# Kernel tuning notes

Hardware: AMD Instinct MI355X
Metric: run time of the kernel (lower is better)

## Reference

```python
import jax, jax.numpy as jnp
import numpy as np

B, N, D, C, NCLS = 8, 2048, 256, 128, 50
EPS = 1e-5  # BatchNorm eps

def _bn(x, g, b):
    # eval-mode BatchNorm1d over channel dim of (B,C,N): running_mean=0, running_var=1
    return x * (g / jnp.sqrt(1.0 + EPS))[:, None] + b[:, None]

def _complex_linear(x, Wr, br, Wi, bi):
    # torch ComplexLinear: complex(fr(x.real)-fi(x.imag), fr(x.imag)+fi(x.real))
    xr, xi = x.real, x.imag
    re = (xr @ Wr.T + br) - (xi @ Wi.T + bi)
    im = (xi @ Wr.T + br) + (xr @ Wi.T + bi)
    return jax.lax.complex(re, im)

def _sa(x, qkW, vW, vb, tW, tb, g, b):
    # x: (B,C,N); q/k share weights (tied in torch), dim C//4
    xq = jnp.einsum('qc,bcn->bnq', qkW, x)            # (B,N,C/4)
    xk = jnp.einsum('qc,bcm->bqm', qkW, x)            # (B,C/4,N)
    energy = jnp.einsum('bnq,bqm->bnm', xq, xk)       # (B,N,N)
    attn = jax.nn.softmax(energy, axis=-1)
    attn = attn / (1e-9 + attn.sum(axis=1, keepdims=True))  # column renorm
    xv = jnp.einsum('oc,bcn->bon', vW, x) + vb[:, None]
    xr = x - jnp.einsum('bcn,bnm->bcm', xv, attn)
    xr = jnp.einsum('oc,bcn->bon', tW, xr) + tb[:, None]
    return x + jax.nn.relu(_bn(xr, g, b))

def reference(xyz, cls_label, A, Bmat, W1r, b1r, W1i, b1i, W2r, b2r, W2i, b2i,
              lbl_emb, ft_w1, ft_g1, ft_b1, ft_w2, ft_g2, ft_b2,
              sa_qk, sa_vw, sa_vb, sa_tw, sa_tb, sa_g, sa_b,
              fuse_w, fuse_g, fuse_b, c1_w, c1_b, bn1_g, bn1_b, c2_w, c2_b):
    pts = xyz.transpose(0, 2, 1)                       # (B,N,3)
    # VecKM(d=256, alpha=30, beta=9): G = eB (eB^H eA), normalized to sqrt(d)
    eA = jnp.exp(1j * (pts @ A))                       # (B,N,D) complex64
    eB = jnp.exp(1j * (pts @ Bmat))
    inner = jnp.einsum('bnd,bne->bde', eB.conj(), eA)  # (B,D,D)
    G = jnp.einsum('bnd,bde->bne', eB, inner)          # (B,N,D)
    G = G / jnp.linalg.norm(G, axis=-1, keepdims=True) * jnp.sqrt(jnp.float32(D))
    G = _complex_linear(G, W1r, b1r, W1i, b1i)
    G = jax.lax.complex(jax.nn.relu(G.real), jax.nn.relu(G.imag))  # ComplexReLU
    G = _complex_linear(G, W2r, b2r, W2i, b2i)
    G = (G.real ** 2 + G.imag ** 2).transpose(0, 2, 1)  # (B,D,N)
    reweight = (cls_label @ lbl_emb)[:, :, None]        # (B,D,1)
    x = G * reweight
    x = jax.nn.relu(_bn(jnp.einsum('oc,bcn->bon', ft_w1, x), ft_g1, ft_b1))
    x = _bn(jnp.einsum('oc,bcn->bon', ft_w2, x), ft_g2, ft_b2)  # (B,C,N)
    feats = []
    for i in range(4):
        x = _sa(x, sa_qk[i], sa_vw[i], sa_vb[i], sa_tw[i], sa_tb[i], sa_g[i], sa_b[i])
        feats.append(x)
    x = jnp.concatenate(feats, axis=1)                  # (B,4C,N)
    x = jax.nn.relu(_bn(jnp.einsum('oc,bcn->bon', fuse_w, x), fuse_g, fuse_b))
    x = jax.nn.relu(_bn(jnp.einsum('oc,bcn->bon', c1_w, x) + c1_b[:, None], bn1_g, bn1_b))
    # dropout is identity in eval mode
    x = jnp.einsum('oc,bcn->bon', c2_w, x) + c2_b[:, None]
    x = jax.nn.log_softmax(x, axis=1)
    return x.transpose(0, 2, 1)                         # (B,N,NCLS)

def setup_inputs():
    key = jax.random.key(0)
    k = jax.random.split(key, 24)
    rn = lambda i, s: jax.random.normal(k[i], s, jnp.float32)
    s = 0.05
    return {
        'xyz': rn(0, (B, 3, N)),
        'cls_label': jax.random.uniform(k[1], (B, 16), jnp.float32),
        'A': rn(2, (3, D)) * 30.0,
        'Bmat': rn(3, (3, D)) * 9.0,
        'W1r': rn(4, (D, D)) * s, 'b1r': rn(5, (D,)) * s,
        'W1i': rn(6, (D, D)) * s, 'b1i': rn(7, (D,)) * s,
        'W2r': rn(8, (D, D)) * s, 'b2r': rn(9, (D,)) * s,
        'W2i': rn(10, (D, D)) * s, 'b2i': rn(11, (D,)) * s,
        'lbl_emb': rn(12, (16, D)),
        'ft_w1': rn(13, (C, D)) * s, 'ft_g1': jnp.ones((C,)), 'ft_b1': jnp.zeros((C,)),
        'ft_w2': rn(14, (C, C)) * s, 'ft_g2': jnp.ones((C,)), 'ft_b2': jnp.zeros((C,)),
        'sa_qk': rn(15, (4, C // 4, C)) * s,
        'sa_vw': rn(16, (4, C, C)) * s, 'sa_vb': rn(17, (4, C)) * s,
        'sa_tw': rn(18, (4, C, C)) * s, 'sa_tb': rn(19, (4, C)) * s,
        'sa_g': jnp.ones((4, C)), 'sa_b': jnp.zeros((4, C)),
        'fuse_w': rn(20, (C, 4 * C)) * s, 'fuse_g': jnp.ones((C,)), 'fuse_b': jnp.zeros((C,)),
        'c1_w': rn(21, (C, C)) * s, 'c1_b': rn(22, (C,)) * s,
        'bn1_g': jnp.ones((C,)), 'bn1_b': jnp.zeros((C,)),
        'c2_w': rn(23, (NCLS, C)) * s, 'c2_b': jnp.zeros((NCLS,)),
    }
```

## Files before the change

### kernel.cpp

```cpp
#include <hip/hip_runtime.h>

#define BB 8
#define NPTS 2048
#define DD 256
#define CCH 128
#define NCLASS 50
#define LOG2E 1.4426950408889634f

typedef __attribute__((ext_vector_type(8))) short short8;
typedef __attribute__((ext_vector_type(4))) float f32x4;
typedef unsigned short u16;
#define MFMA16(a,b,c) __builtin_amdgcn_mfma_f32_16x16x32_bf16(a,b,c,0,0,0)

__device__ __forceinline__ u16 f2bf(float x){
  union { float f; unsigned int u; } v; v.f = x;
  unsigned int r = v.u + 0x7FFFu + ((v.u >> 16) & 1u);
  return (u16)(r >> 16);
}
__device__ __forceinline__ float bf2f(u16 u){
  union { unsigned int u32; float f; } v; v.u32 = ((unsigned int)u) << 16; return v.f;
}
__device__ __forceinline__ void split2(float x, u16& h, u16& l){
  h = f2bf(x); l = f2bf(x - bf2f(h));
}
__device__ __forceinline__ short8 ld8(const u16* p){ return *(const short8*)p; }
__device__ __forceinline__ short8 zero8(){ short8 z = {0,0,0,0,0,0,0,0}; return z; }

struct WSplit {
  const float* src[12];
  int cnt[12];
  int off[12];
};
__global__ __launch_bounds__(256) void wsplit_kernel(WSplit wsp, u16* __restrict__ H,
                                                     u16* __restrict__ L)
{
  int seg = blockIdx.y;
  int idx = blockIdx.x*256 + threadIdx.x;
  if (idx >= wsp.cnt[seg]) return;
  float v = wsp.src[seg][idx];
  u16 h, l; split2(v, h, l);
  H[wsp.off[seg]+idx] = h; L[wsp.off[seg]+idx] = l;
}

__global__ __launch_bounds__(256) void ek1_kernel(
    const float* __restrict__ xyz, const float* __restrict__ A, const float* __restrict__ Bm,
    u16* __restrict__ ATrh, u16* __restrict__ ATrl, u16* __restrict__ ATih, u16* __restrict__ ATil,
    u16* __restrict__ BTrh, u16* __restrict__ BTrl, u16* __restrict__ BTih, u16* __restrict__ BTil)
{
  size_t idx = (size_t)blockIdx.x*256 + threadIdx.x;
  int n = (int)(idx & (NPTS-1));
  int d = (int)((idx >> 11) & (DD-1));
  int b = (int)(idx >> 19);
  float p0 = xyz[((size_t)b*3+0)*NPTS+n];
  float p1 = xyz[((size_t)b*3+1)*NPTS+n];
  float p2 = xyz[((size_t)b*3+2)*NPTS+n];
  float phA = p0*A[d] + p1*A[DD+d] + p2*A[2*DD+d];
  float phB = p0*Bm[d] + p1*Bm[DD+d] + p2*Bm[2*DD+d];
  float sa, ca, sb, cb;
  sincosf(phA, &sa, &ca);
  sincosf(phB, &sb, &cb);
  size_t off = ((size_t)b*DD + d)*NPTS + n;
  u16 h, l;
  split2(ca, h, l); ATrh[off] = h; ATrl[off] = l;
  split2(sa, h, l); ATih[off] = h; ATil[off] = l;
  split2(cb, h, l); BTrh[off] = h; BTrl[off] = l;
  split2(sb, h, l); BTih[off] = h; BTil[off] = l;
}

__global__ __launch_bounds__(256) void ek2_kernel(
    const float* __restrict__ xyz, const float* __restrict__ Bm,
    u16* __restrict__ Brh, u16* __restrict__ Brl, u16* __restrict__ Bih, u16* __restrict__ Bil)
{
  size_t idx = (size_t)blockIdx.x*256 + threadIdx.x;
  int d = (int)(idx & (DD-1));
  int n = (int)((idx >> 8) & (NPTS-1));
  int b = (int)(idx >> 19);
  float p0 = xyz[((size_t)b*3+0)*NPTS+n];
  float p1 = xyz[((size_t)b*3+1)*NPTS+n];
  float p2 = xyz[((size_t)b*3+2)*NPTS+n];
  float phB = p0*Bm[d] + p1*Bm[DD+d] + p2*Bm[2*DD+d];
  float sb, cb;
  sincosf(phB, &sb, &cb);
  size_t off = ((size_t)b*NPTS + n)*DD + d;
  u16 h, l;
  split2(cb, h, l); Brh[off] = h; Brl[off] = l;
  split2(sb, h, l); Bih[off] = h; Bil[off] = l;
}

__global__ __launch_bounds__(256) void inner_mfma_kernel(
    const u16* __restrict__ ATrh, const u16* __restrict__ ATrl,
    const u16* __restrict__ ATih, const u16* __restrict__ ATil,
    const u16* __restrict__ BTrh, const u16* __restrict__ BTrl,
    const u16* __restrict__ BTih, const u16* __restrict__ BTil,
    float2* __restrict__ PART)
{
  int z = blockIdx.z; int b = z & 7; int ch = z >> 3;
  int e0 = blockIdx.y*64, d0 = blockIdx.x*64;
  int tid = threadIdx.x, lane = tid & 63, w = tid >> 6;
  int wr = (w >> 1)*32, wc = (w & 1)*32;
  int r16 = lane & 15, g4 = lane >> 4;
  f32x4 re[2][2] = {}, ip[2][2] = {}, iq[2][2] = {};
  size_t ar_[2], br_[2];
  #pragma unroll
  for (int rg = 0; rg < 2; rg++) {
    ar_[rg] = ((size_t)b*DD + (e0 + wr + rg*16 + r16))*NPTS + g4*8;
    br_[rg] = ((size_t)b*DD + (d0 + wc + rg*16 + r16))*NPTS + g4*8;
  }
  int kbeg = ch*512, kend = kbeg + 512;
  for (int k0 = kbeg; k0 < kend; k0 += 32) {
    short8 arh[2], arl[2], aih[2], ail[2], brh[2], brl[2], bih[2], bil[2];
    #pragma unroll
    for (int rg = 0; rg < 2; rg++) {
      arh[rg] = ld8(ATrh + ar_[rg] + k0); arl[rg] = ld8(ATrl + ar_[rg] + k0);
      aih[rg] = ld8(ATih + ar_[rg] + k0); ail[rg] = ld8(ATil + ar_[rg] + k0);
      brh[rg] = ld8(BTrh + br_[rg] + k0); brl[rg] = ld8(BTrl + br_[rg] + k0);
      bih[rg] = ld8(BTih + br_[rg] + k0); bil[rg] = ld8(BTil + br_[rg] + k0);
    }
    #pragma unroll
    for (int ra = 0; ra < 2; ra++)
      #pragma unroll
      for (int rb = 0; rb < 2; rb++) {
        re[ra][rb] = MFMA16(arh[ra], brh[rb], re[ra][rb]);
        re[ra][rb] = MFMA16(arh[ra], brl[rb], re[ra][rb]);
        re[ra][rb] = MFMA16(arl[ra], brh[rb], re[ra][rb]);
        re[ra][rb] = MFMA16(aih[ra], bih[rb], re[ra][rb]);
        re[ra][rb] = MFMA16(aih[ra], bil[rb], re[ra][rb]);
        re[ra][rb] = MFMA16(ail[ra], bih[rb], re[ra][rb]);
        ip[ra][rb] = MFMA16(aih[ra], brh[rb], ip[ra][rb]);
        ip[ra][rb] = MFMA16(aih[ra], brl[rb], ip[ra][rb]);
        ip[ra][rb] = MFMA16(ail[ra], brh[rb], ip[ra][rb]);
        iq[ra][rb] = MFMA16(arh[ra], bih[rb], iq[ra][rb]);
        iq[ra][rb] = MFMA16(arh[ra], bil[rb], iq[ra][rb]);
        iq[ra][rb] = MFMA16(arl[ra], bih[rb], iq[ra][rb]);
      }
  }
  float2* outp = PART + ((size_t)(ch*BB + b)*DD)*DD;
  #pragma unroll
  for (int ra = 0; ra < 2; ra++)
    #pragma unroll
    for (int rb = 0; rb < 2; rb++)
      #pragma unroll
      for (int j = 0; j < 4; j++) {
        int e = e0 + wr + ra*16 + g4*4 + j;
        int d = d0 + wc + rb*16 + r16;
        outp[(size_t)e*DD + d] = make_float2(re[ra][rb][j], ip[ra][rb][j] - iq[ra][rb][j]);
      }
}

__global__ __launch_bounds__(256) void innred_kernel(const float2* __restrict__ P,
    u16* __restrict__ Irh, u16* __restrict__ Irl, u16* __restrict__ Iih, u16* __restrict__ Iil)
{
  size_t i = (size_t)blockIdx.x*256 + threadIdx.x;
  const size_t S = (size_t)BB*DD*DD;
  float2 a = P[i], b = P[i+S], c = P[i+2*S], d = P[i+3*S];
  float rr = a.x+b.x+c.x+d.x, ii = a.y+b.y+c.y+d.y;
  u16 h, l;
  split2(rr, h, l); Irh[i] = h; Irl[i] = l;
  split2(ii, h, l); Iih[i] = h; Iil[i] = l;
}

__global__ __launch_bounds__(256) void g_mfma_kernel(
    const u16* __restrict__ Brh, const u16* __restrict__ Brl,
    const u16* __restrict__ Bih, const u16* __restrict__ Bil,
    const u16* __restrict__ Irh, const u16* __restrict__ Irl,
    const u16* __restrict__ Iih, const u16* __restrict__ Iil,
    float2* __restrict__ G)
{
  int b = blockIdx.z;
  int n0 = blockIdx.y*64, e0 = blockIdx.x*64;
  int tid = threadIdx.x, lane = tid & 63, w = tid >> 6;
  int wr = (w >> 1)*32, wc = (w & 1)*32;
  int r16 = lane & 15, g4 = lane >> 4;
  f32x4 p[2][2] = {}, q[2][2] = {}, im[2][2] = {};
  size_t ar_[2], br_[2];
  #pragma unroll
  for (int rg = 0; rg < 2; rg++) {
    ar_[rg] = ((size_t)b*NPTS + (n0 + wr + rg*16 + r16))*DD + g4*8;
    br_[rg] = ((size_t)b*DD + (e0 + wc + rg*16 + r16))*DD + g4*8;
  }
  for (int k0 = 0; k0 < DD; k0 += 32) {
    short8 arh[2], arl[2], aih[2], ail[2], brh[2], brl[2], bih[2], bil[2];
    #pragma unroll
    for (int rg = 0; rg < 2; rg++) {
      arh[rg] = ld8(Brh + ar_[rg] + k0); arl[rg] = ld8(Brl + ar_[rg] + k0);
      aih[rg] = ld8(Bih + ar_[rg] + k0); ail[rg] = ld8(Bil + ar_[rg] + k0);
      brh[rg] = ld8(Irh + br_[rg] + k0); brl[rg] = ld8(Irl + br_[rg] + k0);
      bih[rg] = ld8(Iih + br_[rg] + k0); bil[rg] = ld8(Iil + br_[rg] + k0);
    }
    #pragma unroll
    for (int ra = 0; ra < 2; ra++)
      #pragma unroll
      for (int rb = 0; rb < 2; rb++) {
        p[ra][rb] = MFMA16(arh[ra], brh[rb], p[ra][rb]);
        p[ra][rb] = MFMA16(arh[ra], brl[rb], p[ra][rb]);
        p[ra][rb] = MFMA16(arl[ra], brh[rb], p[ra][rb]);
        q[ra][rb] = MFMA16(aih[ra], bih[rb], q[ra][rb]);
        q[ra][rb] = MFMA16(aih[ra], bil[rb], q[ra][rb]);
        q[ra][rb] = MFMA16(ail[ra], bih[rb], q[ra][rb]);
        im[ra][rb] = MFMA16(arh[ra], bih[rb], im[ra][rb]);
        im[ra][rb] = MFMA16(arh[ra], bil[rb], im[ra][rb]);
        im[ra][rb] = MFMA16(arl[ra], bih[rb], im[ra][rb]);
        im[ra][rb] = MFMA16(aih[ra], brh[rb], im[ra][rb]);
        im[ra][rb] = MFMA16(aih[ra], brl[rb], im[ra][rb]);
        im[ra][rb] = MFMA16(ail[ra], brh[rb], im[ra][rb]);
      }
  }
  #pragma unroll
  for (int ra = 0; ra < 2; ra++)
    #pragma unroll
    for (int rb = 0; rb < 2; rb++)
      #pragma unroll
      for (int j = 0; j < 4; j++) {
        int n = n0 + wr + ra*16 + g4*4 + j;
        int e = e0 + wc + rb*16 + r16;
        G[((size_t)b*NPTS + n)*DD + e] = make_float2(p[ra][rb][j] - q[ra][rb][j], im[ra][rb][j]);
      }
}

__global__ __launch_bounds__(256) void gnormsplit_kernel(const float2* __restrict__ Gf,
    u16* __restrict__ Grh, u16* __restrict__ Grl, u16* __restrict__ Gih, u16* __restrict__ Gil)
{
  size_t row = blockIdx.x;
  const float2* p = Gf + row*DD;
  int tid = threadIdx.x;
  float2 v = p[tid];
  __shared__ float red[256];
  red[tid] = v.x*v.x + v.y*v.y;
  __syncthreads();
  for (int w = 128; w > 0; w >>= 1) { if (tid < w) red[tid] += red[tid+w]; __syncthreads(); }
  float sc = 16.f * rsqrtf(red[0]);
  size_t off = row*DD + tid;
  u16 h, l;
  split2(v.x*sc, h, l); Grh[off] = h; Grl[off] = l;
  split2(v.y*sc, h, l); Gih[off] = h; Gil[off] = l;
}

__global__ __launch_bounds__(256) void clinear_mfma_kernel(
    const u16* __restrict__ Arh, const u16* __restrict__ Arl,
    const u16* __restrict__ Aih, const u16* __restrict__ Ail,
    const u16* __restrict__ Wrh, const u16* __restrict__ Wrl,
    const u16* __restrict__ Wih, const u16* __restrict__ Wil,
    const float* __restrict__ br, const float* __restrict__ bi,
    u16* __restrict__ Orh, u16* __restrict__ Orl, u16* __restrict__ Oih, u16* __restrict__ Oil,
    const float* __restrict__ RW, float* __restrict__ GSQ, int mode)
{
  int m0 = blockIdx.y*64, o0 = blockIdx.x*64;
  int tid = threadIdx.x, lane = tid & 63, w = tid >> 6;
  int wr = (w >> 1)*32, wc = (w & 1)*32;
  int r16 = lane & 15, g4 = lane >> 4;
  f32x4 p[2][2] = {}, q[2][2] = {}, im[2][2] = {};
  size_t ar_[2], br_[2];
  #pragma unroll
  for (int rg = 0; rg < 2; rg++) {
    ar_[rg] = (size_t)(m0 + wr + rg*16 + r16)*DD + g4*8;
    br_[rg] = (size_t)(o0 + wc + rg*16 + r16)*DD + g4*8;
  }
  for (int k0 = 0; k0 < DD; k0 += 32) {
    short8 arh[2], arl[2], aih[2], ail[2], brh[2], brl[2], bih[2], bil[2];
    #pragma unroll
    for (int rg = 0; rg < 2; rg++) {
      arh[rg] = ld8(Arh + ar_[rg] + k0); arl[rg] = ld8(Arl + ar_[rg] + k0);
      aih[rg] = ld8(Aih + ar_[rg] + k0); ail[rg] = ld8(Ail + ar_[rg] + k0);
      brh[rg] = ld8(Wrh + br_[rg] + k0); brl[rg] = ld8(Wrl + br_[rg] + k0);
      bih[rg] = ld8(Wih + br_[rg] + k0); bil[rg] = ld8(Wil + br_[rg] + k0);
    }
    #pragma unroll
    for (int ra = 0; ra < 2; ra++)
      #pragma unroll
      for (int rb = 0; rb < 2; rb++) {
        p[ra][rb] = MFMA16(arh[ra], brh[rb], p[ra][rb]);
        p[ra][rb] = MFMA16(arh[ra], brl[rb], p[ra][rb]);
        p[ra][rb] = MFMA16(arl[ra], brh[rb], p[ra][rb]);
        q[ra][rb] = MFMA16(aih[ra], bih[rb], q[ra][rb]);
        q[ra][rb] = MFMA16(aih[ra], bil[rb], q[ra][rb]);
        q[ra][rb] = MFMA16(ail[ra], bih[rb], q[ra][rb]);
        im[ra][rb] = MFMA16(arh[ra], bih[rb], im[ra][rb]);
        im[ra][rb] = MFMA16(arh[ra], bil[rb], im[ra][rb]);
        im[ra][rb] = MFMA16(arl[ra], bih[rb], im[ra][rb]);
        im[ra][rb] = MFMA16(aih[ra], brh[rb], im[ra][rb]);
        im[ra][rb] = MFMA16(aih[ra], brl[rb], im[ra][rb]);
        im[ra][rb] = MFMA16(ail[ra], brh[rb], im[ra][rb]);
      }
  }
  #pragma unroll
  for (int ra = 0; ra < 2; ra++)
    #pragma unroll
    for (int rb = 0; rb < 2; rb++) {
      int o = o0 + wc + rb*16 + r16;
      float brv = br[o], biv = bi[o];
      if (mode == 1) {
        #pragma unroll
        for (int j = 0; j < 4; j++) {
          int m = m0 + wr + ra*16 + g4*4 + j;
          float re = fmaxf(p[ra][rb][j] - q[ra][rb][j] + brv - biv, 0.f);
          float iv = fmaxf(im[ra][rb][j] + brv + biv, 0.f);
          size_t off = (size_t)m*DD + o;
          u16 h, l;
          split2(re, h, l); Orh[off] = h; Orl[off] = l;
          split2(iv, h, l); Oih[off] = h; Oil[off] = l;
        }
      } else {
        int mbase = m0 + wr + ra*16 + g4*4;
        int b = mbase >> 11, nb = mbase & (NPTS-1);
        float rwv = RW[(size_t)b*DD + o];
        float4 gv;
        #pragma unroll
        for (int j = 0; j < 4; j++) {
          float re = p[ra][rb][j] - q[ra][rb][j] + brv - biv;
          float iv = im[ra][rb][j] + brv + biv;
          ((float*)&gv)[j] = (re*re + iv*iv) * rwv;
        }
        *(float4*)(GSQ + ((size_t)b*DD + o)*NPTS + nb) = gv;
      }
    }
}

__global__ void rw_kernel(const float* __restrict__ cls, const float* __restrict__ lbl,
                          float* __restrict__ RW)
{
  int b = blockIdx.x; int d = threadIdx.x;
  float s = 0.f;
  #pragma unroll
  for (int k = 0; k < 16; k++) s += cls[b*16+k] * lbl[k*DD+d];
  RW[b*DD+d] = s;
}

__global__ __launch_bounds__(256) void sgemm_kernel(
    const u16* __restrict__ Wh, const u16* __restrict__ Wl,
    const float* __restrict__ X, float* __restrict__ Y,
    const float* __restrict__ RES,
    const float* __restrict__ bias, const float* __restrict__ bng, const float* __restrict__ bnb,
    u16* __restrict__ YBh, u16* __restrict__ YBl, int ybmode,
    int O, int Cin, size_t xbs, size_t ybs, size_t rbs, int flags)
{
  int b = blockIdx.z;
  int n0 = blockIdx.x*64, o0 = blockIdx.y*64;
  const float* x = X + (size_t)b*xbs;
  __shared__ u16 sXh[64][40], sXl[64][40];
  int tid = threadIdx.x, lane = tid & 63, w = tid >> 6;
  int wo = (w >> 1)*32, wn = (w & 1)*32;
  int r16 = lane & 15, g4 = lane >> 4;
  f32x4 acc[2][2] = {};
  int stc = tid >> 3;
  int stn = (tid & 7)*8;
  for (int k0 = 0; k0 < Cin; k0 += 32) {
    const float* px = x + (size_t)(k0+stc)*NPTS + n0 + stn;
    float4 u0 = *(const float4*)px;
    float4 u1 = *(const float4*)(px+4);
    float v[8] = {u0.x,u0.y,u0.z,u0.w,u1.x,u1.y,u1.z,u1.w};
    __syncthreads();
    #pragma unroll
    for (int j = 0; j < 8; j++) {
      u16 h, l; split2(v[j], h, l);
      sXh[stn+j][stc] = h; sXl[stn+j][stc] = l;
    }
    __syncthreads();
    short8 awh[2], awl[2], bxh[2], bxl[2];
    #pragma unroll
    for (int rg = 0; rg < 2; rg++) {
      int orow = o0 + wo + rg*16 + r16;
      if (orow < O) {
        size_t woff = (size_t)orow*Cin + k0 + g4*8;
        awh[rg] = ld8(Wh + woff); awl[rg] = ld8(Wl + woff);
      } else { awh[rg] = zero8(); awl[rg] = zero8(); }
      bxh[rg] = ld8(&sXh[wn + rg*16 + r16][g4*8]);
      bxl[rg] = ld8(&sXl[wn + rg*16 + r16][g4*8]);
    }
    #pragma unroll
    for (int ra = 0; ra < 2; ra++)
      #pragma unroll
      for (int rb = 0; rb < 2; rb++) {
        acc[ra][rb] = MFMA16(awh[ra], bxh[rb], acc[ra][rb]);
        acc[ra][rb] = MFMA16(awh[ra], bxl[rb], acc[ra][rb]);
        acc[ra][rb] = MFMA16(awl[ra], bxh[rb], acc[ra][rb]);
      }
  }
  #pragma unroll
  for (int ra = 0; ra < 2; ra++)
    #pragma unroll
    for (int rb = 0; rb < 2; rb++)
      #pragma unroll
      for (int j = 0; j < 4; j++) {
        int o = o0 + wo + ra*16 + g4*4 + j;
        if (o >= O) continue;
        int n = n0 + wn + rb*16 + r16;
        float v = acc[ra][rb][j];
        if (flags & 1) v += bias[o];
        if (flags & 2) v = v * (bng[o] * rsqrtf(1.f + 1e-5f)) + bnb[o];
        if (flags & 4) v = fmaxf(v, 0.f);
        if (flags & 8) v += RES[(size_t)b*rbs + (size_t)o*NPTS + n];
        if (ybmode == 0) Y[(size_t)b*ybs + (size_t)o*NPTS + n] = v;
        else if (ybmode == 1) YBh[(size_t)b*ybs + (size_t)o*NPTS + n] = f2bf(v);
        else {
          u16 h, l; split2(v, h, l);
          size_t off = ((size_t)b*NPTS + n)*32 + o;
          YBh[off] = h; YBl[off] = l;
        }
      }
}

__global__ __launch_bounds__(256) void sastat_kernel(
    const u16* __restrict__ Qh, const u16* __restrict__ Ql,
    float* __restrict__ PM, float* __restrict__ PS)
{
  int b = blockIdx.z, ch = blockIdx.y;
  int n0 = blockIdx.x*64;
  size_t base = (size_t)b*NPTS*32;
  int tid = threadIdx.x, lane = tid & 63, wid = tid >> 6;
  int r16 = lane & 15, g4 = lane >> 4;
  size_t ao = base + (size_t)(n0 + wid*16 + r16)*32 + g4*8;
  short8 ah = ld8(Qh + ao), al = ld8(Ql + ao);
  float pm[4] = {-3.4e38f,-3.4e38f,-3.4e38f,-3.4e38f};
  float ps[4] = {0.f,0.f,0.f,0.f};
  int mbeg = ch*512, mend = mbeg + 512;
  for (int mt = mbeg; mt < mend; mt += 32) {
    size_t bo0 = base + (size_t)(mt + r16)*32 + g4*8;
    size_t bo1 = bo0 + 16*32;
    short8 bh0 = ld8(Qh+bo0), bl0 = ld8(Ql+bo0);
    short8 bh1 = ld8(Qh+bo1), bl1 = ld8(Ql+bo1);
    f32x4 a0 = {}, a1 = {};
    a0 = MFMA16(ah, bh0, a0); a0 = MFMA16(ah, bl0, a0); a0 = MFMA16(al, bh0, a0);
    a1 = MFMA16(ah, bh1, a1); a1 = MFMA16(ah, bl1, a1); a1 = MFMA16(al, bh1, a1);
    #pragma unroll
    for (int j = 0; j < 4; j++) {
      float v = fmaxf(a0[j], a1[j]);
      float mn = fmaxf(pm[j], v);
      ps[j] = ps[j]*exp2f((pm[j]-mn)*LOG2E)
            + exp2f((a0[j]-mn)*LOG2E) + exp2f((a1[j]-mn)*LOG2E);
      pm[j] = mn;
    }
  }
  #pragma unroll
  for (int j = 0; j < 4; j++) {
    float m = pm[j], s = ps[j];
    #pragma unroll
    for (int d = 1; d < 16; d <<= 1) {
      float om = __shfl_xor(m, d);
      float os = __shfl_xor(s, d);
      float mn = fmaxf(m, om);
      s = s*exp2f((m-mn)*LOG2E) + os*exp2f((om-mn)*LOG2E);
      m = mn;
    }
    if (r16 == 0) {
      int n_ = n0 + wid*16 + g4*4 + j;
      size_t off = ((size_t)ch*BB + b)*NPTS + n_;
      PM[off] = m; PS[off] = s;
    }
  }
}

__global__ __launch_bounds__(256) void saattn_kernel(
    const u16* __restrict__ Qh, const u16* __restrict__ Ql,
    const float* __restrict__ PM, const float* __restrict__ PS,
    u16* __restrict__ AT, float* __restrict__ CSP)
{
  int b = blockIdx.z, ch = blockIdx.y;
  int m0 = blockIdx.x*64;
  size_t base = (size_t)b*NPTS*32;
  u16* at = AT + (size_t)b*NPTS*NPTS;
  __shared__ u16 lds[4][16][40];
  __shared__ float smx[512], srs[512];
  int tid = threadIdx.x, lane = tid & 63, wid = tid >> 6;
  int r16 = lane & 15, g4 = lane >> 4;
  int nbeg = ch*512, nend = nbeg + 512;
  const size_t S = (size_t)BB*NPTS;
  for (int t = tid; t < 512; t += 256) {
    size_t bn = (size_t)b*NPTS + nbeg + t;
    float m0_ = PM[bn], m1 = PM[S+bn], m2 = PM[2*S+bn], m3 = PM[3*S+bn];
    float mxv = fmaxf(fmaxf(m0_,m1), fmaxf(m2,m3));
    float den = PS[bn]*exp2f((m0_-mxv)*LOG2E) + PS[S+bn]*exp2f((m1-mxv)*LOG2E)
              + PS[2*S+bn]*exp2f((m2-mxv)*LOG2E) + PS[3*S+bn]*exp2f((m3-mxv)*LOG2E);
    smx[t] = mxv; srs[t] = 1.f/den;
  }
  __syncthreads();
  size_t ao = base + (size_t)(m0 + wid*16 + r16)*32 + g4*8;
  short8 ah = ld8(Qh + ao), al = ld8(Ql + ao);
  float csum[4] = {0.f,0.f,0.f,0.f};
  int srow = lane >> 2, soct = (lane & 3)*8;
  for (int nt = nbeg; nt < nend; nt += 32) {
    size_t bo0 = base + (size_t)(nt + r16)*32 + g4*8;
    size_t bo1 = bo0 + 16*32;
    short8 bh0 = ld8(Qh+bo0), bl0 = ld8(Ql+bo0);
    short8 bh1 = ld8(Qh+bo1), bl1 = ld8(Ql+bo1);
    f32x4 a0 = {}, a1 = {};
    a0 = MFMA16(ah, bh0, a0); a0 = MFMA16(ah, bl0, a0); a0 = MFMA16(al, bh0, a0);
    a1 = MFMA16(ah, bh1, a1); a1 = MFMA16(ah, bl1, a1); a1 = MFMA16(al, bh1, a1);
    int nl0 = nt - nbeg + r16, nl1 = nl0 + 16;
    float mx0 = smx[nl0], rs0 = srs[nl0], mx1 = smx[nl1], rs1 = srs[nl1];
    #pragma unroll
    for (int j = 0; j < 4; j++) {
      float t0 = exp2f((a0[j]-mx0)*LOG2E)*rs0;
      float t1 = exp2f((a1[j]-mx1)*LOG2E)*rs1;
      csum[j] += t0 + t1;
      lds[wid][g4*4+j][r16] = f2bf(t0);
      lds[wid][g4*4+j][r16+16] = f2bf(t1);
    }
    __syncthreads();
    short8 row = *(const short8*)&lds[wid][srow][soct];
    *(short8*)(at + (size_t)(m0 + wid*16 + srow)*NPTS + nt + soct) = row;
    __syncthreads();
  }
  #pragma unroll
  for (int j = 0; j < 4; j++) {
    float c = csum[j];
    #pragma unroll
    for (int d = 1; d < 16; d <<= 1) c += __shfl_xor(c, d);
    if (r16 == 0) {
      int m_ = m0 + wid*16 + g4*4 + j;
      CSP[((size_t)ch*BB + b)*NPTS + m_] = c;
    }
  }
}

__global__ __launch_bounds__(256) void apply_mfma_kernel(
    const u16* __restrict__ XV, const u16* __restrict__ AT,
    const float* __restrict__ CSP, const float* __restrict__ XRES, size_t res_bs,
    float* __restrict__ OUT)
{
  int b = blockIdx.z;
  int m0 = blockIdx.x*64;
  int c0 = blockIdx.y*64;
  const u16* xv = XV + (size_t)b*CCH*NPTS;
  const u16* at = AT + (size_t)b*NPTS*NPTS;
  __shared__ float scsi[64];
  int tid = threadIdx.x, lane = tid & 63, w = tid >> 6;
  const size_t S = (size_t)BB*NPTS;
  if (tid < 64) {
    size_t bm = (size_t)b*NPTS + m0 + tid;
    float c = CSP[bm] + CSP[S+bm] + CSP[2*S+bm] + CSP[3*S+bm];
    scsi[tid] = 1.f/(1e-9f + c);
  }
  __syncthreads();
  int wc = c0 + (w >> 1)*32, wm = (w & 1)*32;
  int r16 = lane & 15, g4 = lane >> 4;
  f32x4 acc[2][2] = {};
  const u16* pa0 = xv + (size_t)(wc + r16)*NPTS + g4*8;
  const u16* pa1 = pa0 + (size_t)16*NPTS;
  const u16* pb0 = at + (size_t)(m0 + wm + r16)*NPTS + g4*8;
  const u16* pb1 = pb0 + (size_t)16*NPTS;
  for (int k0 = 0; k0 < NPTS; k0 += 32) {
    short8 a0 = ld8(pa0 + k0);
    short8 a1 = ld8(pa1 + k0);
    short8 b0 = ld8(pb0 + k0);
    short8 b1 = ld8(pb1 + k0);
    acc[0][0] = MFMA16(a0, b0, acc[0][0]);
    acc[0][1] = MFMA16(a0, b1, acc[0][1]);
    acc[1][0] = MFMA16(a1, b0, acc[1][0]);
    acc[1][1] = MFMA16(a1, b1, acc[1][1]);
  }
  #pragma unroll
  for (int ca = 0; ca < 2; ca++)
    #pragma unroll
    for (int mb = 0; mb < 2; mb++) {
      int m = m0 + wm + mb*16 + r16;
      float ci = scsi[wm + mb*16 + r16];
      #pragma unroll
      for (int j = 0; j < 4; j++) {
        int c = wc + ca*16 + g4*4 + j;
        float v = XRES[(size_t)b*res_bs + (size_t)c*NPTS + m] - acc[ca][mb][j]*ci;
        OUT[((size_t)b*CCH + c)*NPTS + m] = v;
      }
    }
}

__global__ __launch_bounds__(256) void lsm_kernel(const float* __restrict__ Y,
                                                  float* __restrict__ OUT)
{
  int idx = blockIdx.x*256 + threadIdx.x;
  int b = idx >> 11, n = idx & (NPTS-1);
  const float* p = Y + (size_t)b*NCLASS*NPTS + n;
  float m = -3.4e38f;
  #pragma unroll
  for (int k = 0; k < NCLASS; k++) m = fmaxf(m, p[(size_t)k*NPTS]);
  float s = 0.f;
  #pragma unroll
  for (int k = 0; k < NCLASS; k++) s += expf(p[(size_t)k*NPTS] - m);
  float L = m + logf(s);
  float* o = OUT + (size_t)idx*NCLASS;
  #pragma unroll
  for (int k = 0; k < NCLASS; k++) o[k] = p[(size_t)k*NPTS] - L;
}

extern "C" void kernel_launch(void* const* d_in, const int* in_sizes, int n_in,
                              void* d_out, int out_size, void* d_ws, size_t ws_size,
                              hipStream_t stream)
{
  (void)in_sizes; (void)n_in; (void)out_size; (void)ws_size;
  const float* xyz  = (const float*)d_in[0];
  const float* cls  = (const float*)d_in[1];
  const float* Amat = (const float*)d_in[2];
  const float* Bm   = (const float*)d_in[3];
  const float* W1r  = (const float*)d_in[4];
  const float* b1r  = (const float*)d_in[5];
  const float* W1i  = (const float*)d_in[6];
  const float* b1i  = (const float*)d_in[7];
  const float* W2r  = (const float*)d_in[8];
  const float* b2r  = (const float*)d_in[9];
  const float* W2i  = (const float*)d_in[10];
  const float* b2i  = (const float*)d_in[11];
  const float* lbl  = (const float*)d_in[12];
  const float* ftw1 = (const float*)d_in[13];
  const float* ftg1 = (const float*)d_in[14];
  const float* ftb1 = (const float*)d_in[15];
  const float* ftw2 = (const float*)d_in[16];
  const float* ftg2 = (const float*)d_in[17];
  const float* ftb2 = (const float*)d_in[18];
  const float* saqk = (const float*)d_in[19];
  const float* savw = (const float*)d_in[20];
  const float* savb = (const float*)d_in[21];
  const float* satw = (const float*)d_in[22];
  const float* satb = (const float*)d_in[23];
  const float* sag  = (const float*)d_in[24];
  const float* sab  = (const float*)d_in[25];
  const float* fusew= (const float*)d_in[26];
  const float* fuseg= (const float*)d_in[27];
  const float* fuseb= (const float*)d_in[28];
  const float* c1w  = (const float*)d_in[29];
  const float* c1b  = (const float*)d_in[30];
  const float* bn1g = (const float*)d_in[31];
  const float* bn1b = (const float*)d_in[32];
  const float* c2w  = (const float*)d_in[33];
  const float* c2b  = (const float*)d_in[34];
  float* out = (float*)d_out;

  float* ws = (float*)d_ws;
  const size_t PS  = (size_t)BB*DD*NPTS;
  const size_t ISZ = (size_t)BB*DD*DD;
  u16* U = (u16*)ws;
  u16 *ATrh = U+0*PS, *ATrl = U+1*PS, *ATih = U+2*PS, *ATil = U+3*PS;
  u16 *BTrh = U+4*PS, *BTrl = U+5*PS, *BTih = U+6*PS, *BTil = U+7*PS;
  u16 *Bnrh = U+8*PS, *Bnrl = U+9*PS, *Bnih = U+10*PS, *Bnil = U+11*PS;
  u16 *Irh = U+12*PS, *Irl = U+12*PS+ISZ, *Iih = U+12*PS+2*ISZ, *Iil = U+12*PS+3*ISZ;
  float* gsq = (float*)(U + 12*PS + 4*ISZ);
  float2* PART = (float2*)gsq;
  float2* Gf = (float2*)ws;
  u16 *G1rh = U+4*PS, *G1rl = U+5*PS, *G1ih = U+6*PS, *G1il = U+7*PS;
  u16 *G2rh = U+8*PS, *G2rl = U+9*PS, *G2ih = U+10*PS, *G2il = U+11*PS;
  u16* attnT = (u16*)ws;
  size_t p = (size_t)BB*NPTS*NPTS;
  float* xfeat = ws + p;  p += (size_t)BB*CCH*NPTS;
  float* feats = ws + p;  p += (size_t)BB*4*CCH*NPTS;
  float* xt1   = ws + p;  p += (size_t)BB*CCH*NPTS;
  float* xt2   = ws + p;  p += (size_t)BB*CCH*NPTS;
  float* ybuf  = ws + p;  p += (size_t)BB*NCLASS*NPTS;
  float* rwb   = ws + p;  p += (size_t)BB*DD;
  float* PMb   = ws + p;  p += (size_t)4*BB*NPTS;
  float* PSb   = ws + p;  p += (size_t)4*BB*NPTS;
  float* CSPb  = ws + p;  p += (size_t)4*BB*NPTS;
  u16* xqh = (u16*)(ws + p);
  u16* xql = xqh + (size_t)BB*NPTS*32;
  u16* xvb = xql + (size_t)BB*NPTS*32;
  u16* wpH = xvb + (size_t)BB*CCH*NPTS;
  u16* wpL = wpH + 557056;

  const int o_w1r=0, o_w1i=65536, o_w2r=131072, o_w2i=196608, o_ft1=262144,
            o_ft2=294912, o_qk=311296, o_vw=327680, o_tw=393216, o_fu=458752,
            o_c1=524288, o_c2=540672;
  WSplit wsp;
  const float* srcs[12] = {W1r,W1i,W2r,W2i,ftw1,ftw2,saqk,savw,satw,fusew,c1w,c2w};
  const int cnts[12] = {65536,65536,65536,65536,32768,16384,16384,65536,65536,65536,16384,6400};
  const int offs[12] = {o_w1r,o_w1i,o_w2r,o_w2i,o_ft1,o_ft2,o_qk,o_vw,o_tw,o_fu,o_c1,o_c2};
  for (int i = 0; i < 12; i++) { wsp.src[i]=srcs[i]; wsp.cnt[i]=cnts[i]; wsp.off[i]=offs[i]; }

  wsplit_kernel<<<dim3(256, 12), 256, 0, stream>>>(wsp, wpH, wpL);
  rw_kernel<<<BB, DD, 0, stream>>>(cls, lbl, rwb);
  ek1_kernel<<<(int)(PS/256), 256, 0, stream>>>(xyz, Amat, Bm,
      ATrh, ATrl, ATih, ATil, BTrh, BTrl, BTih, BTil);
  ek2_kernel<<<(int)(PS/256), 256, 0, stream>>>(xyz, Bm, Bnrh, Bnrl, Bnih, Bnil);
  inner_mfma_kernel<<<dim3(DD/64, DD/64, BB*4), 256, 0, stream>>>(
      ATrh, ATrl, ATih, ATil, BTrh, BTrl, BTih, BTil, PART);
  innred_kernel<<<(int)(ISZ/256), 256, 0, stream>>>(PART, Irh, Irl, Iih, Iil);
  g_mfma_kernel<<<dim3(DD/64, NPTS/64, BB), 256, 0, stream>>>(
      Bnrh, Bnrl, Bnih, Bnil, Irh, Irl, Iih, Iil, Gf);
  gnormsplit_kernel<<<BB*NPTS, 256, 0, stream>>>(Gf, G1rh, G1rl, G1ih, G1il);
  clinear_mfma_kernel<<<dim3(DD/64, (BB*NPTS)/64), 256, 0, stream>>>(
      G1rh, G1rl, G1ih, G1il, wpH+o_w1r, wpL+o_w1r, wpH+o_w1i, wpL+o_w1i,
      b1r, b1i, G2rh, G2rl, G2ih, G2il, nullptr, nullptr, 1);
  clinear_mfma_kernel<<<dim3(DD/64, (BB*NPTS)/64), 256, 0, stream>>>(
      G2rh, G2rl, G2ih, G2il, wpH+o_w2r, wpL+o_w2r, wpH+o_w2i, wpL+o_w2i,
      b2r, b2i, nullptr, nullptr, nullptr, nullptr, rwb, gsq, 2);

  sgemm_kernel<<<dim3(NPTS/64, CCH/64, BB), 256, 0, stream>>>(
      wpH+o_ft1, wpL+o_ft1, gsq, xt1, nullptr, nullptr, ftg1, ftb1, nullptr, nullptr, 0,
      CCH, DD, (size_t)DD*NPTS, (size_t)CCH*NPTS, 0, 2|4);
  sgemm_kernel<<<dim3(NPTS/64, CCH/64, BB), 256, 0, stream>>>(
      wpH+o_ft2, wpL+o_ft2, xt1, xfeat, nullptr, nullptr, ftg2, ftb2, nullptr, nullptr, 0,
      CCH, CCH, (size_t)CCH*NPTS, (size_t)CCH*NPTS, 0, 2);

  const float* xsrc = xfeat;
  size_t xbs = (size_t)CCH*NPTS;
  for (int i = 0; i < 4; i++) {
    sgemm_kernel<<<dim3(NPTS/64, 1, BB), 256, 0, stream>>>(
        wpH+o_qk + i*32*CCH, wpL+o_qk + i*32*CCH, xsrc, nullptr, nullptr,
        nullptr, nullptr, nullptr, xqh, xql, 2, 32, CCH, xbs, 0, 0, 0);
    sastat_kernel<<<dim3(NPTS/64, 4, BB), 256, 0, stream>>>(xqh, xql, PMb, PSb);
    saattn_kernel<<<dim3(NPTS/64, 4, BB), 256, 0, stream>>>(xqh, xql, PMb, PSb, attnT, CSPb);
    sgemm_kernel<<<dim3(NPTS/64, CCH/64, BB), 256, 0, stream>>>(
        wpH+o_vw + i*CCH*CCH, wpL+o_vw + i*CCH*CCH, xsrc, nullptr, nullptr,
        savb + i*CCH, nullptr, nullptr, xvb, nullptr, 1, CCH, CCH, xbs,
        (size_t)CCH*NPTS, 0, 1);
    apply_mfma_kernel<<<dim3(NPTS/64, CCH/64, BB), 256, 0, stream>>>(
        xvb, attnT, CSPb, xsrc, xbs, xt2);
    sgemm_kernel<<<dim3(NPTS/64, CCH/64, BB), 256, 0, stream>>>(
        wpH+o_tw + i*CCH*CCH, wpL+o_tw + i*CCH*CCH, xt2, feats + (size_t)i*CCH*NPTS, xsrc,
        satb + i*CCH, sag + i*CCH, sab + i*CCH, nullptr, nullptr, 0,
        CCH, CCH, (size_t)CCH*NPTS, (size_t)4*CCH*NPTS, xbs, 1|2|4|8);
    xsrc = feats + (size_t)i*CCH*NPTS;
    xbs = (size_t)4*CCH*NPTS;
  }

  sgemm_kernel<<<dim3(NPTS/64, CCH/64, BB), 256, 0, stream>>>(
      wpH+o_fu, wpL+o_fu, feats, xt1, nullptr, nullptr, fuseg, fuseb, nullptr, nullptr, 0,
      CCH, 4*CCH, (size_t)4*CCH*NPTS, (size_t)CCH*NPTS, 0, 2|4);
  sgemm_kernel<<<dim3(NPTS/64, CCH/64, BB), 256, 0, stream>>>(
      wpH+o_c1, wpL+o_c1, xt1, xt2, nullptr, c1b, bn1g, bn1b, nullptr, nullptr, 0,
      CCH, CCH, (size_t)CCH*NPTS, (size_t)CCH*NPTS, 0, 1|2|4);
  sgemm_kernel<<<dim3(NPTS/64, 1, BB), 256, 0, stream>>>(
      wpH+o_c2, wpL+o_c2, xt2, ybuf, nullptr, c2b, nullptr, nullptr, nullptr, nullptr, 0,
      NCLASS, CCH, (size_t)CCH*NPTS, (size_t)NCLASS*NPTS, 0, 1);
  lsm_kernel<<<(BB*NPTS)/256, 256, 0, stream>>>(ybuf, out);
}
```

Before: 998.7 us.

## Fuse attention probability generation with PV product and remap clinear tiles per XCD

```diff
diff --git a/kernel.cpp b/kernel.cpp
--- a/kernel.cpp
+++ b/kernel.cpp
@@ -106,8 +106,10 @@
     ar_[rg] = ((size_t)b*DD + (e0 + wr + rg*16 + r16))*NPTS + g4*8;
     br_[rg] = ((size_t)b*DD + (d0 + wc + rg*16 + r16))*NPTS + g4*8;
   }
-  int kbeg = ch*512, kend = kbeg + 512;
-  for (int k0 = kbeg; k0 < kend; k0 += 32) {
+  int kbeg = ch*512;
+  #pragma unroll 2
+  for (int kk = 0; kk < 512; kk += 32) {
+    int k0 = kbeg + kk;
     short8 arh[2], arl[2], aih[2], ail[2], brh[2], brl[2], bih[2], bil[2];
     #pragma unroll
     for (int rg = 0; rg < 2; rg++) {
@@ -178,6 +180,7 @@
     ar_[rg] = ((size_t)b*NPTS + (n0 + wr + rg*16 + r16))*DD + g4*8;
     br_[rg] = ((size_t)b*DD + (e0 + wc + rg*16 + r16))*DD + g4*8;
   }
+  #pragma unroll
   for (int k0 = 0; k0 < DD; k0 += 32) {
     short8 arh[2], arl[2], aih[2], ail[2], brh[2], brl[2], bih[2], bil[2];
     #pragma unroll
@@ -244,7 +247,10 @@
     u16* __restrict__ Orh, u16* __restrict__ Orl, u16* __restrict__ Oih, u16* __restrict__ Oil,
     const float* __restrict__ RW, float* __restrict__ GSQ, int mode)
 {
-  int m0 = blockIdx.y*64, o0 = blockIdx.x*64;
+  int wg = blockIdx.y * gridDim.x + blockIdx.x;
+  int xcd = wg & 7, idx = wg >> 3;
+  int o0 = (idx & 3) * 64;
+  int m0 = (xcd * ((int)gridDim.y >> 3) + (idx >> 2)) * 64;
   int tid = threadIdx.x, lane = tid & 63, w = tid >> 6;
   int wr = (w >> 1)*32, wc = (w & 1)*32;
   int r16 = lane & 15, g4 = lane >> 4;
@@ -255,6 +261,7 @@
     ar_[rg] = (size_t)(m0 + wr + rg*16 + r16)*DD + g4*8;
     br_[rg] = (size_t)(o0 + wc + rg*16 + r16)*DD + g4*8;
   }
+  #pragma unroll
   for (int k0 = 0; k0 < DD; k0 += 32) {
     short8 arh[2], arl[2], aih[2], ail[2], brh[2], brl[2], bih[2], bil[2];
     #pragma unroll
@@ -449,114 +456,95 @@
   }
 }
 
-__global__ __launch_bounds__(256) void saattn_kernel(
+__global__ __launch_bounds__(256) void comb1_kernel(
+    const float* __restrict__ PM, const float* __restrict__ PS,
+    float* __restrict__ MX, float* __restrict__ RS)
+{
+  size_t i = (size_t)blockIdx.x*256 + threadIdx.x;
+  const size_t S = (size_t)BB*NPTS;
+  float m0 = PM[i], m1 = PM[i+S], m2 = PM[i+2*S], m3 = PM[i+3*S];
+  float mx = fmaxf(fmaxf(m0,m1), fmaxf(m2,m3));
+  float den = PS[i]*exp2f((m0-mx)*LOG2E) + PS[i+S]*exp2f((m1-mx)*LOG2E)
+            + PS[i+2*S]*exp2f((m2-mx)*LOG2E) + PS[i+3*S]*exp2f((m3-mx)*LOG2E);
+  MX[i] = mx; RS[i] = 1.f/den;
+}
+
+__global__ __launch_bounds__(512) void fused_pv_kernel(
     const u16* __restrict__ Qh, const u16* __restrict__ Ql,
-    const float* __restrict__ PM, const float* __restrict__ PS,
-    u16* __restrict__ AT, float* __restrict__ CSP)
-{
-  int b = blockIdx.z, ch = blockIdx.y;
+    const float* __restrict__ MX, const float* __restrict__ RS,
+    const u16* __restrict__ XV, const float* __restrict__ XRES, size_t res_bs,
+    float* __restrict__ OUT)
+{
+  int b = blockIdx.y;
   int m0 = blockIdx.x*64;
-  size_t base = (size_t)b*NPTS*32;
-  u16* at = AT + (size_t)b*NPTS*NPTS;
-  __shared__ u16 lds[4][16][40];
-  __shared__ float smx[512], srs[512];
-  int tid = threadIdx.x, lane = tid & 63, wid = tid >> 6;
+  size_t qbase = (size_t)b*NPTS*32;
+  const u16* xv = XV + (size_t)b*CCH*NPTS;
+  __shared__ float smx[NPTS], srs[NPTS];
+  __shared__ u16 Pl[64][36];
+  __shared__ float csacc[64];
+  int tid = threadIdx.x, lane = tid & 63, w = tid >> 6;
   int r16 = lane & 15, g4 = lane >> 4;
-  int nbeg = ch*512, nend = nbeg + 512;
-  const size_t S = (size_t)BB*NPTS;
-  for (int t = tid; t < 512; t += 256) {
-    size_t bn = (size_t)b*NPTS + nbeg + t;
-    float m0_ = PM[bn], m1 = PM[S+bn], m2 = PM[2*S+bn], m3 = PM[3*S+bn];
-    float mxv = fmaxf(fmaxf(m0_,m1), fmaxf(m2,m3));
-    float den = PS[bn]*exp2f((m0_-mxv)*LOG2E) + PS[S+bn]*exp2f((m1-mxv)*LOG2E)
-              + PS[2*S+bn]*exp2f((m2-mxv)*LOG2E) + PS[3*S+bn]*exp2f((m3-mxv)*LOG2E);
-    smx[t] = mxv; srs[t] = 1.f/den;
-  }
+  for (int t = tid; t < NPTS; t += 512) {
+    smx[t] = MX[(size_t)b*NPTS + t];
+    srs[t] = RS[(size_t)b*NPTS + t];
+  }
+  if (tid < 64) csacc[tid] = 0.f;
+  int ma = w >> 1, na = w & 1;
+  int cw = (w >> 1)*32, mw = (w & 1)*32;
+  size_t eao = qbase + (size_t)(m0 + ma*16 + r16)*32 + g4*8;
+  short8 eah = ld8(Qh + eao), eal = ld8(Ql + eao);
+  const u16* pa0 = xv + (size_t)(cw + r16)*NPTS + g4*8;
+  const u16* pa1 = pa0 + (size_t)16*NPTS;
+  f32x4 acc[2][2] = {};
+  float cs[4] = {0.f,0.f,0.f,0.f};
+  size_t ebo = qbase + (size_t)(na*16 + r16)*32 + g4*8;
+  short8 ebh = ld8(Qh + ebo), ebl = ld8(Ql + ebo);
+  short8 xa0 = ld8(pa0), xa1 = ld8(pa1);
   __syncthreads();
-  size_t ao = base + (size_t)(m0 + wid*16 + r16)*32 + g4*8;
-  short8 ah = ld8(Qh + ao), al = ld8(Ql + ao);
-  float csum[4] = {0.f,0.f,0.f,0.f};
-  int srow = lane >> 2, soct = (lane & 3)*8;
-  for (int nt = nbeg; nt < nend; nt += 32) {
-    size_t bo0 = base + (size_t)(nt + r16)*32 + g4*8;
-    size_t bo1 = bo0 + 16*32;
-    short8 bh0 = ld8(Qh+bo0), bl0 = ld8(Ql+bo0);
-    short8 bh1 = ld8(Qh+bo1), bl1 = ld8(Ql+bo1);
-    f32x4 a0 = {}, a1 = {};
-    a0 = MFMA16(ah, bh0, a0); a0 = MFMA16(ah, bl0, a0); a0 = MFMA16(al, bh0, a0);
-    a1 = MFMA16(ah, bh1, a1); a1 = MFMA16(ah, bl1, a1); a1 = MFMA16(al, bh1, a1);
-    int nl0 = nt - nbeg + r16, nl1 = nl0 + 16;
-    float mx0 = smx[nl0], rs0 = srs[nl0], mx1 = smx[nl1], rs1 = srs[nl1];
+  for (int nt = 0; nt < NPTS; nt += 32) {
+    f32x4 e = {};
+    e = MFMA16(eah, ebh, e); e = MFMA16(eah, ebl, e); e = MFMA16(eal, ebh, e);
+    int nn = nt + na*16 + r16;
+    float mxv_ = smx[nn], rsv_ = srs[nn];
     #pragma unroll
     for (int j = 0; j < 4; j++) {
-      float t0 = exp2f((a0[j]-mx0)*LOG2E)*rs0;
-      float t1 = exp2f((a1[j]-mx1)*LOG2E)*rs1;
-      csum[j] += t0 + t1;
-      lds[wid][g4*4+j][r16] = f2bf(t0);
-      lds[wid][g4*4+j][r16+16] = f2bf(t1);
+      float t = exp2f((e[j]-mxv_)*LOG2E)*rsv_;
+      cs[j] += t;
+      Pl[ma*16 + g4*4 + j][na*16 + r16] = f2bf(t);
+    }
+    short8 nebh = zero8(), nebl = zero8(), nxa0 = zero8(), nxa1 = zero8();
+    if (nt + 32 < NPTS) {
+      size_t ebo2 = qbase + (size_t)(nt + 32 + na*16 + r16)*32 + g4*8;
+      nebh = ld8(Qh + ebo2); nebl = ld8(Ql + ebo2);
+      nxa0 = ld8(pa0 + nt + 32); nxa1 = ld8(pa1 + nt + 32);
     }
     __syncthreads();
-    short8 row = *(const short8*)&lds[wid][srow][soct];
-    *(short8*)(at + (size_t)(m0 + wid*16 + srow)*NPTS + nt + soct) = row;
+    short8 b0 = *(const short8*)&Pl[mw + r16][g4*8];
+    short8 b1 = *(const short8*)&Pl[mw + 16 + r16][g4*8];
+    acc[0][0] = MFMA16(xa0, b0, acc[0][0]);
+    acc[0][1] = MFMA16(xa0, b1, acc[0][1]);
+    acc[1][0] = MFMA16(xa1, b0, acc[1][0]);
+    acc[1][1] = MFMA16(xa1, b1, acc[1][1]);
     __syncthreads();
+    ebh = nebh; ebl = nebl; xa0 = nxa0; xa1 = nxa1;
   }
   #pragma unroll
   for (int j = 0; j < 4; j++) {
-    float c = csum[j];
+    float c = cs[j];
     #pragma unroll
     for (int d = 1; d < 16; d <<= 1) c += __shfl_xor(c, d);
-    if (r16 == 0) {
-      int m_ = m0 + wid*16 + g4*4 + j;
-      CSP[((size_t)ch*BB + b)*NPTS + m_] = c;
-    }
-  }
-}
-
-__global__ __launch_bounds__(256) void apply_mfma_kernel(
-    const u16* __restrict__ XV, const u16* __restrict__ AT,
-    const float* __restrict__ CSP, const float* __restrict__ XRES, size_t res_bs,
-    float* __restrict__ OUT)
-{
-  int b = blockIdx.z;
-  int m0 = blockIdx.x*64;
-  int c0 = blockIdx.y*64;
-  const u16* xv = XV + (size_t)b*CCH*NPTS;
-  const u16* at = AT + (size_t)b*NPTS*NPTS;
-  __shared__ float scsi[64];
-  int tid = threadIdx.x, lane = tid & 63, w = tid >> 6;
-  const size_t S = (size_t)BB*NPTS;
-  if (tid < 64) {
-    size_t bm = (size_t)b*NPTS + m0 + tid;
-    float c = CSP[bm] + CSP[S+bm] + CSP[2*S+bm] + CSP[3*S+bm];
-    scsi[tid] = 1.f/(1e-9f + c);
+    if (r16 == 0) atomicAdd(&csacc[ma*16 + g4*4 + j], c);
   }
   __syncthreads();
-  int wc = c0 + (w >> 1)*32, wm = (w & 1)*32;
-  int r16 = lane & 15, g4 = lane >> 4;
-  f32x4 acc[2][2] = {};
-  const u16* pa0 = xv + (size_t)(wc + r16)*NPTS + g4*8;
-  const u16* pa1 = pa0 + (size_t)16*NPTS;
-  const u16* pb0 = at + (size_t)(m0 + wm + r16)*NPTS + g4*8;
-  const u16* pb1 = pb0 + (size_t)16*NPTS;
-  for (int k0 = 0; k0 < NPTS; k0 += 32) {
-    short8 a0 = ld8(pa0 + k0);
-    short8 a1 = ld8(pa1 + k0);
-    short8 b0 = ld8(pb0 + k0);
-    short8 b1 = ld8(pb1 + k0);
-    acc[0][0] = MFMA16(a0, b0, acc[0][0]);
-    acc[0][1] = MFMA16(a0, b1, acc[0][1]);
-    acc[1][0] = MFMA16(a1, b0, acc[1][0]);
-    acc[1][1] = MFMA16(a1, b1, acc[1][1]);
-  }
   #pragma unroll
   for (int ca = 0; ca < 2; ca++)
     #pragma unroll
     for (int mb = 0; mb < 2; mb++) {
-      int m = m0 + wm + mb*16 + r16;
-      float ci = scsi[wm + mb*16 + r16];
+      int m = m0 + mw + mb*16 + r16;
+      float ci = 1.f/(1e-9f + csacc[mw + mb*16 + r16]);
       #pragma unroll
       for (int j = 0; j < 4; j++) {
-        int c = wc + ca*16 + g4*4 + j;
+        int c = cw + ca*16 + g4*4 + j;
         float v = XRES[(size_t)b*res_bs + (size_t)c*NPTS + m] - acc[ca][mb][j]*ci;
         OUT[((size_t)b*CCH + c)*NPTS + m] = v;
       }
@@ -636,7 +624,6 @@
   float2* Gf = (float2*)ws;
   u16 *G1rh = U+4*PS, *G1rl = U+5*PS, *G1ih = U+6*PS, *G1il = U+7*PS;
   u16 *G2rh = U+8*PS, *G2rl = U+9*PS, *G2ih = U+10*PS, *G2il = U+11*PS;
-  u16* attnT = (u16*)ws;
   size_t p = (size_t)BB*NPTS*NPTS;
   float* xfeat = ws + p;  p += (size_t)BB*CCH*NPTS;
   float* feats = ws + p;  p += (size_t)BB*4*CCH*NPTS;
@@ -644,9 +631,10 @@
   float* xt2   = ws + p;  p += (size_t)BB*CCH*NPTS;
   float* ybuf  = ws + p;  p += (size_t)BB*NCLASS*NPTS;
   float* rwb   = ws + p;  p += (size_t)BB*DD;
+  float* mxv   = ws + p;  p += (size_t)BB*NPTS;
+  float* rsv   = ws + p;  p += (size_t)BB*NPTS;
   float* PMb   = ws + p;  p += (size_t)4*BB*NPTS;
   float* PSb   = ws + p;  p += (size_t)4*BB*NPTS;
-  float* CSPb  = ws + p;  p += (size_t)4*BB*NPTS;
   u16* xqh = (u16*)(ws + p);
   u16* xql = xqh + (size_t)BB*NPTS*32;
   u16* xvb = xql + (size_t)BB*NPTS*32;
@@ -694,13 +682,13 @@
         wpH+o_qk + i*32*CCH, wpL+o_qk + i*32*CCH, xsrc, nullptr, nullptr,
         nullptr, nullptr, nullptr, xqh, xql, 2, 32, CCH, xbs, 0, 0, 0);
     sastat_kernel<<<dim3(NPTS/64, 4, BB), 256, 0, stream>>>(xqh, xql, PMb, PSb);
-    saattn_kernel<<<dim3(NPTS/64, 4, BB), 256, 0, stream>>>(xqh, xql, PMb, PSb, attnT, CSPb);
+    comb1_kernel<<<(BB*NPTS)/256, 256, 0, stream>>>(PMb, PSb, mxv, rsv);
     sgemm_kernel<<<dim3(NPTS/64, CCH/64, BB), 256, 0, stream>>>(
         wpH+o_vw + i*CCH*CCH, wpL+o_vw + i*CCH*CCH, xsrc, nullptr, nullptr,
         savb + i*CCH, nullptr, nullptr, xvb, nullptr, 1, CCH, CCH, xbs,
         (size_t)CCH*NPTS, 0, 1);
-    apply_mfma_kernel<<<dim3(NPTS/64, CCH/64, BB), 256, 0, stream>>>(
-        xvb, attnT, CSPb, xsrc, xbs, xt2);
+    fused_pv_kernel<<<dim3(NPTS/64, BB), 512, 0, stream>>>(
+        xqh, xql, mxv, rsv, xvb, xsrc, xbs, xt2);
     sgemm_kernel<<<dim3(NPTS/64, CCH/64, BB), 256, 0, stream>>>(
         wpH+o_tw + i*CCH*CCH, wpL+o_tw + i*CCH*CCH, xt2, feats + (size_t)i*CCH*NPTS, xsrc,
         satb + i*CCH, sag + i*CCH, sab + i*CCH, nullptr, nullptr, 0,
```

Result: faster. 970.5 us (-2.8%).
